# Performance work log

Hardware: AMD Instinct MI355X
Metric: run time of the kernel (lower is better)

## Reference

```python
import jax, jax.numpy as jnp
import numpy as np

N_NODES = 100000


def _gcn_propagate(x, src, dst, n):
    """Symmetric-normalized propagation with self-loops (PyG gcn_norm, K=1).

    out[dst] += deg^-1/2[src] * deg^-1/2[dst] * x[src], including self-loops.
    """
    loop = jnp.arange(n, dtype=src.dtype)
    s = jnp.concatenate([src, loop])
    d = jnp.concatenate([dst, loop])
    deg = jax.ops.segment_sum(jnp.ones_like(d, dtype=x.dtype), d, num_segments=n)
    dinv = jnp.where(deg > 0, jax.lax.rsqrt(deg), jnp.zeros_like(deg))
    norm = dinv[s] * dinv[d]            # [E+N]
    msg = x[s] * norm[:, None]          # [E+N, F] gathered messages
    return jax.ops.segment_sum(msg, d, num_segments=n)


def setup_inputs() -> dict:
    key = jax.random.key(0)
    ks = jax.random.split(key, 6)
    n, e, f, h, c = N_NODES, 1600000, 64, 64, 16
    x = jax.random.normal(ks[0], (n, f), dtype=jnp.float32)
    edge_index = jax.random.randint(ks[1], (2, e), 0, n, dtype=jnp.int64)
    W1 = jax.random.normal(ks[2], (h, f), dtype=jnp.float32) * 0.1
    b1 = jnp.zeros((h,), dtype=jnp.float32)
    W2 = jax.random.normal(ks[3], (h, h), dtype=jnp.float32) * 0.1
    b2 = jnp.zeros((h,), dtype=jnp.float32)
    W3 = jax.random.normal(ks[4], (c, h), dtype=jnp.float32) * 0.1
    b3 = jnp.zeros((c,), dtype=jnp.float32)
    return {"x": x, "edge_index": edge_index, "W1": W1, "b1": b1,
            "W2": W2, "b2": b2, "W3": W3, "b3": b3}


def reference(x, edge_index, W1, b1, W2, b2, W3, b3):
    n = x.shape[0]
    src, dst = edge_index[0], edge_index[1]
    # SGConv 1 (K=1): propagate then linear; dropout is identity in eval mode
    h = _gcn_propagate(x, src, dst, n) @ W1.T + b1
    h = jax.nn.relu(h)
    # SGConv 2
    h = _gcn_propagate(h, src, dst, n) @ W2.T + b2
    h = jax.nn.relu(h)
    # final linear
    return h @ W3.T + b3
```

## Files before the change

kernel.cpp:

```cpp
#include <hip/hip_runtime.h>
#include <hip/hip_fp16.h>


#define F 64
#define C 16
#define SCAN_B 1024

__device__ __forceinline__ float rl(float v, int l) {
    return __uint_as_float(__builtin_amdgcn_readlane(__float_as_uint(v), l));
}

__device__ __forceinline__ float4 ld_h4(const float2* base, size_t idx) {
    float2 raw = base[idx];
    __half2 lo = __builtin_bit_cast(__half2, raw.x);
    __half2 hi = __builtin_bit_cast(__half2, raw.y);
    float2 f0 = __half22float2(lo);
    float2 f1 = __half22float2(hi);
    return make_float4(f0.x, f0.y, f1.x, f1.y);
}

__global__ void degrank_kernel(const int* __restrict__ dst, int* __restrict__ deg,
                               int* __restrict__ rank, int E) {
    int i = (blockIdx.x * blockDim.x + threadIdx.x) * 4;
    if (i + 4 <= E) {
        int4 d = *(const int4*)(dst + i);
        rank[i]     = atomicAdd(&deg[d.x], 1);
        rank[i + 1] = atomicAdd(&deg[d.y], 1);
        rank[i + 2] = atomicAdd(&deg[d.z], 1);
        rank[i + 3] = atomicAdd(&deg[d.w], 1);
    } else {
        for (int k = i; k < E; ++k) rank[k] = atomicAdd(&deg[dst[k]], 1);
    }
}

__global__ __launch_bounds__(256) void scan1_kernel(const int* __restrict__ deg,
                                                    int* __restrict__ part,
                                                    int* __restrict__ bsum, int n) {
    __shared__ int ts[256];
    int b = blockIdx.x, t = threadIdx.x;
    int base = b * SCAN_B + t * 4;
    int v[4], sum = 0;
#pragma unroll
    for (int k = 0; k < 4; ++k) { int i = base + k; v[k] = (i < n) ? deg[i] : 0; sum += v[k]; }
    ts[t] = sum;
    __syncthreads();
    for (int off = 1; off < 256; off <<= 1) {
        int add = (t >= off) ? ts[t - off] : 0;
        __syncthreads();
        ts[t] += add;
        __syncthreads();
    }
    int run = ts[t] - sum;
#pragma unroll
    for (int k = 0; k < 4; ++k) { int i = base + k; if (i < n) part[i] = run; run += v[k]; }
    if (t == 255) bsum[b] = ts[255];
}

__global__ __launch_bounds__(256) void scan2_kernel(int* __restrict__ bsum, int nb) {
    __shared__ int ts[256];
    int t = threadIdx.x;
    int v = (t < nb) ? bsum[t] : 0;
    ts[t] = v;
    __syncthreads();
    for (int off = 1; off < 256; off <<= 1) {
        int add = (t >= off) ? ts[t - off] : 0;
        __syncthreads();
        ts[t] += add;
        __syncthreads();
    }
    if (t < nb) bsum[t] = ts[t] - v;
}

__global__ void scan3_kernel(const int* __restrict__ part, const int* __restrict__ bsum,
                             const int* __restrict__ deg, int* __restrict__ rowptr,
                             float* __restrict__ dinv, int n, int E) {
    int i = blockIdx.x * blockDim.x + threadIdx.x;
    if (i < n) {
        rowptr[i] = part[i] + bsum[i / SCAN_B];
        dinv[i] = rsqrtf((float)deg[i] + 1.0f);
    }
    if (i == 0) rowptr[n] = E;
}

__global__ void fill_kernel(const int* __restrict__ src, const int* __restrict__ dst,
                            const int* __restrict__ rank, const int* __restrict__ rowptr,
                            int* __restrict__ csr_src, int E) {
    int i = (blockIdx.x * blockDim.x + threadIdx.x) * 4;
    if (i + 4 <= E) {
        int4 s = *(const int4*)(src + i);
        int4 d = *(const int4*)(dst + i);
        int4 r = *(const int4*)(rank + i);
        csr_src[rowptr[d.x] + r.x] = s.x;
        csr_src[rowptr[d.y] + r.y] = s.y;
        csr_src[rowptr[d.z] + r.z] = s.z;
        csr_src[rowptr[d.w] + r.w] = s.w;
    } else {
        for (int k = i; k < E; ++k) csr_src[rowptr[dst[k]] + rank[k]] = src[k];
    }
}

template <bool SCALE>
__global__ __launch_bounds__(256) void gemm_kernel(
    const float4* __restrict__ in4, const float* __restrict__ W,
    const float* __restrict__ scale, __half* __restrict__ yout, int n) {
    int tid = threadIdx.x;
    int lane = tid & 63;
    int m = lane & 15;
    float4 w[16];
#pragma unroll
    for (int t = 0; t < 16; ++t) w[t] = *(const float4*)(W + (size_t)lane * F + 4 * t);
    int gw = blockIdx.x * 4 + (tid >> 6);
    int nw = gridDim.x * 4;
    int node = gw;
    if (node >= n) return;
    float4 v = in4[(size_t)node * 16 + m];
    while (true) {
        int nxt = node + nw;
        float4 vn;
        if (nxt < n) vn = in4[(size_t)nxt * 16 + m];
        float acc = 0.0f;
#pragma unroll
        for (int t = 0; t < 16; ++t) {
            acc = fmaf(rl(v.x, t), w[t].x, acc);
            acc = fmaf(rl(v.y, t), w[t].y, acc);
            acc = fmaf(rl(v.z, t), w[t].z, acc);
            acc = fmaf(rl(v.w, t), w[t].w, acc);
        }
        if (SCALE) acc *= scale[node];
        yout[(size_t)node * F + lane] = __float2half(acc);
        if (nxt >= n) break;
        v = vn;
        node = nxt;
    }
}

__global__ __launch_bounds__(256) void gather1_kernel(
    const float2* __restrict__ y4, const int* __restrict__ rowptr,
    const int* __restrict__ csr_src, const float* __restrict__ dinv,
    const float* __restrict__ b1, float* __restrict__ h1s, int n) {
    int tid = threadIdx.x;
    int lane = tid & 63;
    int q = lane >> 4, m = lane & 15;
    float4 bias = *(const float4*)(b1 + 4 * m);
    int gw = blockIdx.x * 4 + (tid >> 6);
    int nw = gridDim.x * 4;
    for (int node = gw; node < n; node += nw) {
        int beg = rowptr[node], end = rowptr[node + 1];
        float4 a0 = {0, 0, 0, 0}, a1 = {0, 0, 0, 0}, a2 = {0, 0, 0, 0}, a3 = {0, 0, 0, 0};
        int p = beg;
        for (; p + 16 <= end; p += 16) {
            int s0 = csr_src[p + q];
            int s1 = csr_src[p + 4 + q];
            int s2 = csr_src[p + 8 + q];
            int s3 = csr_src[p + 12 + q];
            float4 v0 = ld_h4(y4, (size_t)s0 * 16 + m);
            float4 v1 = ld_h4(y4, (size_t)s1 * 16 + m);
            float4 v2 = ld_h4(y4, (size_t)s2 * 16 + m);
            float4 v3 = ld_h4(y4, (size_t)s3 * 16 + m);
            a0.x += v0.x; a0.y += v0.y; a0.z += v0.z; a0.w += v0.w;
            a1.x += v1.x; a1.y += v1.y; a1.z += v1.z; a1.w += v1.w;
            a2.x += v2.x; a2.y += v2.y; a2.z += v2.z; a2.w += v2.w;
            a3.x += v3.x; a3.y += v3.y; a3.z += v3.z; a3.w += v3.w;
        }
        for (; p < end; p += 4) {
            int idx = p + q;
            if (idx < end) {
                int s = csr_src[idx];
                float4 v = ld_h4(y4, (size_t)s * 16 + m);
                a0.x += v.x; a0.y += v.y; a0.z += v.z; a0.w += v.w;
            }
        }
        a0.x += a1.x + a2.x + a3.x;
        a0.y += a1.y + a2.y + a3.y;
        a0.z += a1.z + a2.z + a3.z;
        a0.w += a1.w + a2.w + a3.w;
        a0.x += __shfl_xor(a0.x, 16); a0.y += __shfl_xor(a0.y, 16);
        a0.z += __shfl_xor(a0.z, 16); a0.w += __shfl_xor(a0.w, 16);
        a0.x += __shfl_xor(a0.x, 32); a0.y += __shfl_xor(a0.y, 32);
        a0.z += __shfl_xor(a0.z, 32); a0.w += __shfl_xor(a0.w, 32);
        float dd = dinv[node];
        float4 self = ld_h4(y4, (size_t)node * 16 + m);
        if (q == 0) {
            float4 r;
            r.x = dd * fmaxf(fmaf(dd, a0.x + self.x, bias.x), 0.0f);
            r.y = dd * fmaxf(fmaf(dd, a0.y + self.y, bias.y), 0.0f);
            r.z = dd * fmaxf(fmaf(dd, a0.z + self.z, bias.z), 0.0f);
            r.w = dd * fmaxf(fmaf(dd, a0.w + self.w, bias.w), 0.0f);
            *(float4*)(h1s + (size_t)node * F + 4 * m) = r;
        }
    }
}

__global__ __launch_bounds__(256) void gather2_kernel(
    const float2* __restrict__ y4, const int* __restrict__ rowptr,
    const int* __restrict__ csr_src, const float* __restrict__ dinv,
    const float* __restrict__ b2, const float* __restrict__ W3,
    const float* __restrict__ b3, float* __restrict__ out, int n) {
    int tid = threadIdx.x;
    int lane = tid & 63;
    int q = lane >> 4, m = lane & 15;
    float4 bias = *(const float4*)(b2 + 4 * m);
    float4 w3[4];
#pragma unroll
    for (int t = 0; t < 4; ++t)
        w3[t] = *(const float4*)(W3 + (size_t)m * F + 16 * q + 4 * t);
    float b3r = b3[m];
    int gw = blockIdx.x * 4 + (tid >> 6);
    int nw = gridDim.x * 4;
    for (int node = gw; node < n; node += nw) {
        int beg = rowptr[node], end = rowptr[node + 1];
        float4 a0 = {0, 0, 0, 0}, a1 = {0, 0, 0, 0}, a2 = {0, 0, 0, 0}, a3 = {0, 0, 0, 0};
        int p = beg;
        for (; p + 16 <= end; p += 16) {
            int s0 = csr_src[p + q];
            int s1 = csr_src[p + 4 + q];
            int s2 = csr_src[p + 8 + q];
            int s3 = csr_src[p + 12 + q];
            float4 v0 = ld_h4(y4, (size_t)s0 * 16 + m);
            float4 v1 = ld_h4(y4, (size_t)s1 * 16 + m);
            float4 v2 = ld_h4(y4, (size_t)s2 * 16 + m);
            float4 v3 = ld_h4(y4, (size_t)s3 * 16 + m);
            a0.x += v0.x; a0.y += v0.y; a0.z += v0.z; a0.w += v0.w;
            a1.x += v1.x; a1.y += v1.y; a1.z += v1.z; a1.w += v1.w;
            a2.x += v2.x; a2.y += v2.y; a2.z += v2.z; a2.w += v2.w;
            a3.x += v3.x; a3.y += v3.y; a3.z += v3.z; a3.w += v3.w;
        }
        for (; p < end; p += 4) {
            int idx = p + q;
            if (idx < end) {
                int s = csr_src[idx];
                float4 v = ld_h4(y4, (size_t)s * 16 + m);
                a0.x += v.x; a0.y += v.y; a0.z += v.z; a0.w += v.w;
            }
        }
        a0.x += a1.x + a2.x + a3.x;
        a0.y += a1.y + a2.y + a3.y;
        a0.z += a1.z + a2.z + a3.z;
        a0.w += a1.w + a2.w + a3.w;
        a0.x += __shfl_xor(a0.x, 16); a0.y += __shfl_xor(a0.y, 16);
        a0.z += __shfl_xor(a0.z, 16); a0.w += __shfl_xor(a0.w, 16);
        a0.x += __shfl_xor(a0.x, 32); a0.y += __shfl_xor(a0.y, 32);
        a0.z += __shfl_xor(a0.z, 32); a0.w += __shfl_xor(a0.w, 32);
        float dd = dinv[node];
        float4 self = ld_h4(y4, (size_t)node * 16 + m);
        float4 h;
        h.x = fmaxf(fmaf(dd, a0.x + self.x, bias.x), 0.0f);
        h.y = fmaxf(fmaf(dd, a0.y + self.y, bias.y), 0.0f);
        h.z = fmaxf(fmaf(dd, a0.z + self.z, bias.z), 0.0f);
        h.w = fmaxf(fmaf(dd, a0.w + self.w, bias.w), 0.0f);
        float partial = 0.0f;
#pragma unroll
        for (int t = 0; t < 4; ++t) {
            int sl = 4 * q + t;
            partial = fmaf(__shfl(h.x, sl), w3[t].x, partial);
            partial = fmaf(__shfl(h.y, sl), w3[t].y, partial);
            partial = fmaf(__shfl(h.z, sl), w3[t].z, partial);
            partial = fmaf(__shfl(h.w, sl), w3[t].w, partial);
        }
        partial += __shfl_xor(partial, 16);
        partial += __shfl_xor(partial, 32);
        if (q == 0) out[(size_t)node * C + m] = partial + b3r;
    }
}

extern "C" void kernel_launch(void* const* d_in, const int* in_sizes, int n_in,
                              void* d_out, int out_size, void* d_ws, size_t ws_size,
                              hipStream_t stream) {
    const float* x  = (const float*)d_in[0];
    const int* edge = (const int*)d_in[1];
    const float* W1 = (const float*)d_in[2];
    const float* b1 = (const float*)d_in[3];
    const float* W2 = (const float*)d_in[4];
    const float* b2 = (const float*)d_in[5];
    const float* W3 = (const float*)d_in[6];
    const float* b3 = (const float*)d_in[7];
    float* out = (float*)d_out;

    int n = in_sizes[0] / F;
    int E = in_sizes[1] / 2;
    const int* src = edge;
    const int* dst = edge + E;

    int nb = (n + SCAN_B - 1) / SCAN_B;

    char* ws = (char*)d_ws;
    size_t o = 0;
    auto alloc = [&](size_t bytes) { char* p = ws + o; o += (bytes + 255) & ~(size_t)255; return p; };
    int*    deg     = (int*)   alloc((size_t)n * 4);
    int*    rank    = (int*)   alloc((size_t)E * 4);
    int*    part    = (int*)   alloc((size_t)n * 4);
    int*    bsum    = (int*)   alloc(256 * 4);
    int*    rowptr  = (int*)   alloc((size_t)(n + 1) * 4);
    int*    csr_src = (int*)   alloc((size_t)E * 4);
    float*  dinv    = (float*) alloc((size_t)n * 4);
    __half* y1      = (__half*)alloc((size_t)n * F * 2);
    float*  h1s     = (float*) alloc((size_t)n * F * 4);
    __half* y2      = y1;

    hipMemsetAsync(deg, 0, (size_t)n * 4, stream);
    degrank_kernel<<<(E / 4 + 255) / 256, 256, 0, stream>>>(dst, deg, rank, E);

    scan1_kernel<<<nb, 256, 0, stream>>>(deg, part, bsum, n);
    scan2_kernel<<<1, 256, 0, stream>>>(bsum, nb);
    scan3_kernel<<<(n + 255) / 256, 256, 0, stream>>>(part, bsum, deg, rowptr, dinv, n, E);

    gemm_kernel<true><<<2048, 256, 0, stream>>>((const float4*)x, W1, dinv, y1, n);

    fill_kernel<<<(E / 4 + 255) / 256, 256, 0, stream>>>(src, dst, rank, rowptr, csr_src, E);

    gather1_kernel<<<2048, 256, 0, stream>>>(
        (const float2*)y1, rowptr, csr_src, dinv, b1, h1s, n);

    gemm_kernel<false><<<2048, 256, 0, stream>>>((const float4*)h1s, W2, nullptr, y2, n);

    gather2_kernel<<<2048, 256, 0, stream>>>(
        (const float2*)y2, rowptr, csr_src, dinv, b2, W3, b3, out, n);
}
```

Baseline: 300.5 us.

## Assign one 16-lane quarter-wave per node in gather kernels instead of full wave

```diff
diff --git a/kernel.cpp b/kernel.cpp
--- a/kernel.cpp
+++ b/kernel.cpp
@@ -5,10 +5,6 @@
 #define F 64
 #define C 16
 #define SCAN_B 1024
-
-__device__ __forceinline__ float rl(float v, int l) {
-    return __uint_as_float(__builtin_amdgcn_readlane(__float_as_uint(v), l));
-}
 
 __device__ __forceinline__ float4 ld_h4(const float2* base, size_t idx) {
     float2 raw = base[idx];
@@ -17,6 +13,10 @@
     float2 f0 = __half22float2(lo);
     float2 f1 = __half22float2(hi);
     return make_float4(f0.x, f0.y, f1.x, f1.y);
+}
+
+__device__ __forceinline__ float rl(float v, int l) {
+    return __uint_as_float(__builtin_amdgcn_readlane(__float_as_uint(v), l));
 }
 
 __global__ void degrank_kernel(const int* __restrict__ dst, int* __restrict__ deg,
@@ -135,131 +135,142 @@
 }
 
 __global__ __launch_bounds__(256) void gather1_kernel(
-    const float2* __restrict__ y4, const int* __restrict__ rowptr,
+    const float2* __restrict__ y, const int* __restrict__ rowptr,
     const int* __restrict__ csr_src, const float* __restrict__ dinv,
     const float* __restrict__ b1, float* __restrict__ h1s, int n) {
     int tid = threadIdx.x;
-    int lane = tid & 63;
-    int q = lane >> 4, m = lane & 15;
+    int m = tid & 15;
     float4 bias = *(const float4*)(b1 + 4 * m);
-    int gw = blockIdx.x * 4 + (tid >> 6);
-    int nw = gridDim.x * 4;
-    for (int node = gw; node < n; node += nw) {
+    int qid = (blockIdx.x * 256 + tid) >> 4;
+    int nq = (gridDim.x * 256) >> 4;
+    for (int node = qid; node < n; node += nq) {
         int beg = rowptr[node], end = rowptr[node + 1];
         float4 a0 = {0, 0, 0, 0}, a1 = {0, 0, 0, 0}, a2 = {0, 0, 0, 0}, a3 = {0, 0, 0, 0};
         int p = beg;
-        for (; p + 16 <= end; p += 16) {
-            int s0 = csr_src[p + q];
-            int s1 = csr_src[p + 4 + q];
-            int s2 = csr_src[p + 8 + q];
-            int s3 = csr_src[p + 12 + q];
-            float4 v0 = ld_h4(y4, (size_t)s0 * 16 + m);
-            float4 v1 = ld_h4(y4, (size_t)s1 * 16 + m);
-            float4 v2 = ld_h4(y4, (size_t)s2 * 16 + m);
-            float4 v3 = ld_h4(y4, (size_t)s3 * 16 + m);
+        for (; p + 8 <= end; p += 8) {
+            int s0 = csr_src[p],     s1 = csr_src[p + 1];
+            int s2 = csr_src[p + 2], s3 = csr_src[p + 3];
+            int s4 = csr_src[p + 4], s5 = csr_src[p + 5];
+            int s6 = csr_src[p + 6], s7 = csr_src[p + 7];
+            float4 v0 = ld_h4(y, (size_t)s0 * 16 + m);
+            float4 v1 = ld_h4(y, (size_t)s1 * 16 + m);
+            float4 v2 = ld_h4(y, (size_t)s2 * 16 + m);
+            float4 v3 = ld_h4(y, (size_t)s3 * 16 + m);
+            float4 v4 = ld_h4(y, (size_t)s4 * 16 + m);
+            float4 v5 = ld_h4(y, (size_t)s5 * 16 + m);
+            float4 v6 = ld_h4(y, (size_t)s6 * 16 + m);
+            float4 v7 = ld_h4(y, (size_t)s7 * 16 + m);
+            a0.x += v0.x + v4.x; a0.y += v0.y + v4.y; a0.z += v0.z + v4.z; a0.w += v0.w + v4.w;
+            a1.x += v1.x + v5.x; a1.y += v1.y + v5.y; a1.z += v1.z + v5.z; a1.w += v1.w + v5.w;
+            a2.x += v2.x + v6.x; a2.y += v2.y + v6.y; a2.z += v2.z + v6.z; a2.w += v2.w + v6.w;
+            a3.x += v3.x + v7.x; a3.y += v3.y + v7.y; a3.z += v3.z + v7.z; a3.w += v3.w + v7.w;
+        }
+        if (p + 4 <= end) {
+            int s0 = csr_src[p], s1 = csr_src[p + 1], s2 = csr_src[p + 2], s3 = csr_src[p + 3];
+            float4 v0 = ld_h4(y, (size_t)s0 * 16 + m);
+            float4 v1 = ld_h4(y, (size_t)s1 * 16 + m);
+            float4 v2 = ld_h4(y, (size_t)s2 * 16 + m);
+            float4 v3 = ld_h4(y, (size_t)s3 * 16 + m);
             a0.x += v0.x; a0.y += v0.y; a0.z += v0.z; a0.w += v0.w;
             a1.x += v1.x; a1.y += v1.y; a1.z += v1.z; a1.w += v1.w;
             a2.x += v2.x; a2.y += v2.y; a2.z += v2.z; a2.w += v2.w;
             a3.x += v3.x; a3.y += v3.y; a3.z += v3.z; a3.w += v3.w;
-        }
-        for (; p < end; p += 4) {
-            int idx = p + q;
-            if (idx < end) {
-                int s = csr_src[idx];
-                float4 v = ld_h4(y4, (size_t)s * 16 + m);
-                a0.x += v.x; a0.y += v.y; a0.z += v.z; a0.w += v.w;
-            }
+            p += 4;
+        }
+        for (; p < end; ++p) {
+            int s = csr_src[p];
+            float4 v = ld_h4(y, (size_t)s * 16 + m);
+            a0.x += v.x; a0.y += v.y; a0.z += v.z; a0.w += v.w;
         }
         a0.x += a1.x + a2.x + a3.x;
         a0.y += a1.y + a2.y + a3.y;
         a0.z += a1.z + a2.z + a3.z;
         a0.w += a1.w + a2.w + a3.w;
-        a0.x += __shfl_xor(a0.x, 16); a0.y += __shfl_xor(a0.y, 16);
-        a0.z += __shfl_xor(a0.z, 16); a0.w += __shfl_xor(a0.w, 16);
-        a0.x += __shfl_xor(a0.x, 32); a0.y += __shfl_xor(a0.y, 32);
-        a0.z += __shfl_xor(a0.z, 32); a0.w += __shfl_xor(a0.w, 32);
         float dd = dinv[node];
-        float4 self = ld_h4(y4, (size_t)node * 16 + m);
-        if (q == 0) {
-            float4 r;
-            r.x = dd * fmaxf(fmaf(dd, a0.x + self.x, bias.x), 0.0f);
-            r.y = dd * fmaxf(fmaf(dd, a0.y + self.y, bias.y), 0.0f);
-            r.z = dd * fmaxf(fmaf(dd, a0.z + self.z, bias.z), 0.0f);
-            r.w = dd * fmaxf(fmaf(dd, a0.w + self.w, bias.w), 0.0f);
-            *(float4*)(h1s + (size_t)node * F + 4 * m) = r;
-        }
+        float4 self = ld_h4(y, (size_t)node * 16 + m);
+        float4 r;
+        r.x = dd * fmaxf(fmaf(dd, a0.x + self.x, bias.x), 0.0f);
+        r.y = dd * fmaxf(fmaf(dd, a0.y + self.y, bias.y), 0.0f);
+        r.z = dd * fmaxf(fmaf(dd, a0.z + self.z, bias.z), 0.0f);
+        r.w = dd * fmaxf(fmaf(dd, a0.w + self.w, bias.w), 0.0f);
+        *(float4*)(h1s + (size_t)node * F + 4 * m) = r;
     }
 }
 
 __global__ __launch_bounds__(256) void gather2_kernel(
-    const float2* __restrict__ y4, const int* __restrict__ rowptr,
+    const float2* __restrict__ y, const int* __restrict__ rowptr,
     const int* __restrict__ csr_src, const float* __restrict__ dinv,
     const float* __restrict__ b2, const float* __restrict__ W3,
     const float* __restrict__ b3, float* __restrict__ out, int n) {
     int tid = threadIdx.x;
     int lane = tid & 63;
-    int q = lane >> 4, m = lane & 15;
+    int m = lane & 15;
+    int qbase = lane & 48;
     float4 bias = *(const float4*)(b2 + 4 * m);
-    float4 w3[4];
-#pragma unroll
-    for (int t = 0; t < 4; ++t)
-        w3[t] = *(const float4*)(W3 + (size_t)m * F + 16 * q + 4 * t);
     float b3r = b3[m];
-    int gw = blockIdx.x * 4 + (tid >> 6);
-    int nw = gridDim.x * 4;
-    for (int node = gw; node < n; node += nw) {
+    int qid = (blockIdx.x * 256 + tid) >> 4;
+    int nq = (gridDim.x * 256) >> 4;
+    for (int node = qid; node < n; node += nq) {
         int beg = rowptr[node], end = rowptr[node + 1];
         float4 a0 = {0, 0, 0, 0}, a1 = {0, 0, 0, 0}, a2 = {0, 0, 0, 0}, a3 = {0, 0, 0, 0};
         int p = beg;
-        for (; p + 16 <= end; p += 16) {
-            int s0 = csr_src[p + q];
-            int s1 = csr_src[p + 4 + q];
-            int s2 = csr_src[p + 8 + q];
-            int s3 = csr_src[p + 12 + q];
-            float4 v0 = ld_h4(y4, (size_t)s0 * 16 + m);
-            float4 v1 = ld_h4(y4, (size_t)s1 * 16 + m);
-            float4 v2 = ld_h4(y4, (size_t)s2 * 16 + m);
-            float4 v3 = ld_h4(y4, (size_t)s3 * 16 + m);
+        for (; p + 8 <= end; p += 8) {
+            int s0 = csr_src[p],     s1 = csr_src[p + 1];
+            int s2 = csr_src[p + 2], s3 = csr_src[p + 3];
+            int s4 = csr_src[p + 4], s5 = csr_src[p + 5];
+            int s6 = csr_src[p + 6], s7 = csr_src[p + 7];
+            float4 v0 = ld_h4(y, (size_t)s0 * 16 + m);
+            float4 v1 = ld_h4(y, (size_t)s1 * 16 + m);
+            float4 v2 = ld_h4(y, (size_t)s2 * 16 + m);
+            float4 v3 = ld_h4(y, (size_t)s3 * 16 + m);
+            float4 v4 = ld_h4(y, (size_t)s4 * 16 + m);
+            float4 v5 = ld_h4(y, (size_t)s5 * 16 + m);
+            float4 v6 = ld_h4(y, (size_t)s6 * 16 + m);
+            float4 v7 = ld_h4(y, (size_t)s7 * 16 + m);
+            a0.x += v0.x + v4.x; a0.y += v0.y + v4.y; a0.z += v0.z + v4.z; a0.w += v0.w + v4.w;
+            a1.x += v1.x + v5.x; a1.y += v1.y + v5.y; a1.z += v1.z + v5.z; a1.w += v1.w + v5.w;
+            a2.x += v2.x + v6.x; a2.y += v2.y + v6.y; a2.z += v2.z + v6.z; a2.w += v2.w + v6.w;
+            a3.x += v3.x + v7.x; a3.y += v3.y + v7.y; a3.z += v3.z + v7.z; a3.w += v3.w + v7.w;
+        }
+        if (p + 4 <= end) {
+            int s0 = csr_src[p], s1 = csr_src[p + 1], s2 = csr_src[p + 2], s3 = csr_src[p + 3];
+            float4 v0 = ld_h4(y, (size_t)s0 * 16 + m);
+            float4 v1 = ld_h4(y, (size_t)s1 * 16 + m);
+            float4 v2 = ld_h4(y, (size_t)s2 * 16 + m);
+            float4 v3 = ld_h4(y, (size_t)s3 * 16 + m);
             a0.x += v0.x; a0.y += v0.y; a0.z += v0.z; a0.w += v0.w;
             a1.x += v1.x; a1.y += v1.y; a1.z += v1.z; a1.w += v1.w;
             a2.x += v2.x; a2.y += v2.y; a2.z += v2.z; a2.w += v2.w;
             a3.x += v3.x; a3.y += v3.y; a3.z += v3.z; a3.w += v3.w;
-        }
-        for (; p < end; p += 4) {
-            int idx = p + q;
-            if (idx < end) {
-                int s = csr_src[idx];
-                float4 v = ld_h4(y4, (size_t)s * 16 + m);
-                a0.x += v.x; a0.y += v.y; a0.z += v.z; a0.w += v.w;
-            }
+            p += 4;
+        }
+        for (; p < end; ++p) {
+            int s = csr_src[p];
+            float4 v = ld_h4(y, (size_t)s * 16 + m);
+            a0.x += v.x; a0.y += v.y; a0.z += v.z; a0.w += v.w;
         }
         a0.x += a1.x + a2.x + a3.x;
         a0.y += a1.y + a2.y + a3.y;
         a0.z += a1.z + a2.z + a3.z;
         a0.w += a1.w + a2.w + a3.w;
-        a0.x += __shfl_xor(a0.x, 16); a0.y += __shfl_xor(a0.y, 16);
-        a0.z += __shfl_xor(a0.z, 16); a0.w += __shfl_xor(a0.w, 16);
-        a0.x += __shfl_xor(a0.x, 32); a0.y += __shfl_xor(a0.y, 32);
-        a0.z += __shfl_xor(a0.z, 32); a0.w += __shfl_xor(a0.w, 32);
         float dd = dinv[node];
-        float4 self = ld_h4(y4, (size_t)node * 16 + m);
+        float4 self = ld_h4(y, (size_t)node * 16 + m);
         float4 h;
         h.x = fmaxf(fmaf(dd, a0.x + self.x, bias.x), 0.0f);
         h.y = fmaxf(fmaf(dd, a0.y + self.y, bias.y), 0.0f);
         h.z = fmaxf(fmaf(dd, a0.z + self.z, bias.z), 0.0f);
         h.w = fmaxf(fmaf(dd, a0.w + self.w, bias.w), 0.0f);
-        float partial = 0.0f;
-#pragma unroll
-        for (int t = 0; t < 4; ++t) {
-            int sl = 4 * q + t;
-            partial = fmaf(__shfl(h.x, sl), w3[t].x, partial);
-            partial = fmaf(__shfl(h.y, sl), w3[t].y, partial);
-            partial = fmaf(__shfl(h.z, sl), w3[t].z, partial);
-            partial = fmaf(__shfl(h.w, sl), w3[t].w, partial);
-        }
-        partial += __shfl_xor(partial, 16);
-        partial += __shfl_xor(partial, 32);
-        if (q == 0) out[(size_t)node * C + m] = partial + b3r;
+        float acc = 0.0f;
+#pragma unroll
+        for (int t = 0; t < 16; ++t) {
+            float4 wv = *(const float4*)(W3 + (size_t)m * F + 4 * t);
+            float hx = __shfl(h.x, qbase + t);
+            float hy = __shfl(h.y, qbase + t);
+            float hz = __shfl(h.z, qbase + t);
+            float hw = __shfl(h.w, qbase + t);
+            acc = fmaf(hx, wv.x, fmaf(hy, wv.y, fmaf(hz, wv.z, fmaf(hw, wv.w, acc))));
+        }
+        out[(size_t)node * C + m] = acc + b3r;
     }
 }
 
```

Result: faster. 283.5 us (-5.7%).
